# Kernel tuning notes

Measured on AMD Instinct MI355X. Metric: run time of the kernel, lower is better.

The kernel has to match this reference:

```python
import jax, jax.numpy as jnp
import numpy as np

B, H, W, N = 4, 64, 64, 64
NEAR, FAR = 2.0, 6.0
HID = 64


def setup_inputs() -> dict:
    key = jax.random.key(0)
    ks = jax.random.split(key, 6)
    ray_origins = jnp.tile(jnp.array([0.0, 0.0, 4.0], jnp.float32), (B, H, W, 1))
    ray_directions = jax.random.normal(ks[0], (B, H, W, 3), jnp.float32)
    tform_cam2world = jnp.eye(4, dtype=jnp.float32) + 0.1 * jax.random.normal(ks[1], (B, 4, 4), jnp.float32)
    depth_noise = jax.random.uniform(ks[2], (B, H, W, N), jnp.float32)
    u_samples = jax.random.uniform(ks[3], (B, H, W, N), jnp.float32)
    W1 = 0.5 * jax.random.normal(ks[4], (3, HID), jnp.float32)
    b1 = jnp.zeros((HID,), jnp.float32)
    W2 = 0.5 * jax.random.normal(ks[5], (HID, 4), jnp.float32)
    b2 = jnp.zeros((4,), jnp.float32)
    return dict(ray_origins=ray_origins, ray_directions=ray_directions,
                tform_cam2world=tform_cam2world, depth_noise=depth_noise,
                u_samples=u_samples, W1=W1, b1=b1, W2=W2, b2=b2)


def field(pts, W1, b1, W2, b2):
    # tiny radiance-field MLP standing in for the generator's sampler
    h = jax.nn.relu(pts @ W1 + b1)
    out = h @ W2 + b2
    sigma = out[..., 0]
    rgb = jax.nn.sigmoid(out[..., 1:4])
    return sigma, rgb


def compositing_weights(sigma, z_vals):
    # alpha-compositing weights (render_volume_density)
    dists = jnp.concatenate([z_vals[..., 1:] - z_vals[..., :-1],
                             jnp.full_like(z_vals[..., :1], 1e10)], axis=-1)
    alpha = 1.0 - jnp.exp(-jax.nn.relu(sigma) * dists)
    trans = jnp.cumprod(1.0 - alpha + 1e-10, axis=-1)
    trans = jnp.concatenate([jnp.ones_like(trans[..., :1]), trans[..., :-1]], axis=-1)
    return alpha * trans


def sample_pdf(bins, weights, u):
    # bins [R, M+1], weights [R, M], u [R, S] -> samples [R, S]
    pdf = weights / jnp.sum(weights, axis=-1, keepdims=True)
    cdf = jnp.cumsum(pdf, axis=-1)
    cdf = jnp.concatenate([jnp.zeros_like(cdf[..., :1]), cdf], axis=-1)  # [R, M+1]
    inds = jax.vmap(lambda c, uu: jnp.searchsorted(c, uu, side='right'))(cdf, u)
    last = cdf.shape[-1] - 1
    below = jnp.clip(inds - 1, 0, last)
    above = jnp.clip(inds, 0, last)
    cdf_b = jnp.take_along_axis(cdf, below, axis=-1)
    cdf_a = jnp.take_along_axis(cdf, above, axis=-1)
    bin_b = jnp.take_along_axis(bins, below, axis=-1)
    bin_a = jnp.take_along_axis(bins, above, axis=-1)
    denom = cdf_a - cdf_b
    denom = jnp.where(denom < 1e-5, 1.0, denom)
    t = (u - cdf_b) / denom
    return bin_b + t * (bin_a - bin_b)


def reference(ray_origins, ray_directions, tform_cam2world, depth_noise, u_samples, W1, b1, W2, b2):
    rd = ray_directions / jnp.linalg.norm(ray_directions, axis=-1, keepdims=True)
    # stratified coarse samples along each ray
    t = (jnp.arange(N, dtype=jnp.float32) + depth_noise) / N           # [B,H,W,N]
    z_vals = NEAR + (FAR - NEAR) * t
    pts = ray_origins[..., None, :] + rd[..., None, :] * z_vals[..., None]
    sigma, rgb = field(pts, W1, b1, W2, b2)                            # [B,H,W,N], [B,H,W,N,3]

    # --- hierarchical importance sampling (no_grad in original) ---
    w = compositing_weights(sigma, z_vals).reshape(-1, N)              # [R,N]
    pad = jnp.pad(w, ((0, 0), (1, 1)), constant_values=-jnp.inf)
    mx = jnp.maximum(pad[:, :-1], pad[:, 1:])                          # max_pool1d(k=2,s=1,p=1) -> [R,N+1]
    sm = 0.5 * (mx[:, :-1] + mx[:, 1:]) + 0.01                        # avg_pool1d(k=2,s=1)  -> [R,N]
    z_mid = (0.5 * (z_vals[..., 1:] + z_vals[..., :-1])).reshape(-1, N - 1)
    z_samples = sample_pdf(z_mid, sm[:, 1:-1], u_samples.reshape(-1, N))
    z_samples = jax.lax.stop_gradient(z_samples.reshape(B, H, W, N))

    # fine evaluation + merge-sort of coarse/fine samples
    z_all = jnp.concatenate([z_vals, z_samples], axis=-1)              # [B,H,W,2N]
    idx = jnp.argsort(z_all, axis=-1)
    z_sorted = jnp.take_along_axis(z_all, idx, axis=-1)
    pts_f = ray_origins[..., None, :] + rd[..., None, :] * z_samples[..., None]
    sigma_f, rgb_f = field(pts_f, W1, b1, W2, b2)
    sigma_all = jnp.take_along_axis(jnp.concatenate([sigma, sigma_f], axis=-1), idx, axis=-1)
    rgb_cat = jnp.concatenate([rgb, rgb_f], axis=-2)
    rgb_all = jnp.take_along_axis(rgb_cat, jnp.broadcast_to(idx[..., None], idx.shape + (3,)), axis=-2)

    # final alpha compositing
    w_all = compositing_weights(sigma_all, z_sorted)
    rgb_pred = jnp.sum(w_all[..., None] * rgb_all, axis=-2)            # [B,H,W,3]
    depth_pred = jnp.sum(w_all * z_sorted, axis=-1)                    # [B,H,W]
    mask_pred = jnp.sum(w_all, axis=-1)                                # [B,H,W]

    # camera-space depth (invert_space: R_w2c = R^T)
    R_w2c = jnp.swapaxes(tform_cam2world[:, :3, :3], -1, -2)           # [B,3,3]
    view_dir = jnp.einsum('bhwj,bij->bhwi', rd, R_w2c)
    depth_cam = -(view_dir * depth_pred[..., None])[..., -1]
    return rgb_pred, depth_cam, mask_pred
```

## Files before the change

kernel.cpp:

```cpp
#include <hip/hip_runtime.h>
#include <hip/hip_bf16.h>
#include <math.h>

#define Nn    64
#define RPB   2
#define NRAYS 16384
#define NEARV 2.0f
#define FARV  6.0f

typedef __attribute__((ext_vector_type(8))) short bf16x8;
typedef __attribute__((ext_vector_type(4))) float f32x4;
typedef __attribute__((ext_vector_type(2))) float f32x2;

template <int CTRL, int RMASK>
__device__ __forceinline__ float dpp_mv(float x, float ident) {
  return __int_as_float(__builtin_amdgcn_update_dpp(
      __float_as_int(ident), __float_as_int(x), CTRL, RMASK, 0xf, false));
}
__device__ __forceinline__ float shfl_up1(float x) {
  return __int_as_float(__builtin_amdgcn_update_dpp(
      __float_as_int(x), __float_as_int(x), 0x138, 0xf, 0xf, false));
}
__device__ __forceinline__ float shfl_dn1(float x) {
  return __int_as_float(__builtin_amdgcn_update_dpp(
      __float_as_int(x), __float_as_int(x), 0x130, 0xf, 0xf, false));
}
__device__ __forceinline__ float scan_add_dpp(float x) {
  x += dpp_mv<0x111, 0xf>(x, 0.f);
  x += dpp_mv<0x112, 0xf>(x, 0.f);
  x += dpp_mv<0x114, 0xf>(x, 0.f);
  x += dpp_mv<0x118, 0xf>(x, 0.f);
  x += dpp_mv<0x142, 0xa>(x, 0.f);
  x += dpp_mv<0x143, 0xc>(x, 0.f);
  return x;
}
__device__ __forceinline__ float scan_mul_dpp(float x) {
  x *= dpp_mv<0x111, 0xf>(x, 1.f);
  x *= dpp_mv<0x112, 0xf>(x, 1.f);
  x *= dpp_mv<0x114, 0xf>(x, 1.f);
  x *= dpp_mv<0x118, 0xf>(x, 1.f);
  x *= dpp_mv<0x142, 0xa>(x, 1.f);
  x *= dpp_mv<0x143, 0xc>(x, 1.f);
  return x;
}
__device__ __forceinline__ float reduce_add_bcast(float x) {
  x = scan_add_dpp(x);
  return __int_as_float(__builtin_amdgcn_readlane(__float_as_int(x), 63));
}

__device__ __forceinline__ float fast_rcp(float x) { return __builtin_amdgcn_rcpf(x); }
__device__ __forceinline__ float sigmoidf_fast(float x) { return fast_rcp(1.f + __expf(-x)); }

__device__ __forceinline__ short bfhi_bits(float x) { return (short)(__float_as_uint(x) >> 16); }
__device__ __forceinline__ float bfhi_val(float x)  { return __uint_as_float(__float_as_uint(x) & 0xFFFF0000u); }

template <int LEVEL, int D>
__device__ __forceinline__ void bitonic_stage(unsigned& k, int lane) {
  unsigned t;
  if constexpr (D == 32) {
    t = (unsigned)__builtin_amdgcn_ds_bpermute((lane ^ 32) << 2, (int)k);
  } else {
    t = (unsigned)__builtin_amdgcn_ds_swizzle((int)k, (D << 10) | 0x1F);
  }
  const bool bitd = (lane & D) != 0;
  const bool desc = (lane & (1 << LEVEL)) != 0;
  const unsigned mn = (k < t) ? k : t;
  const unsigned mx = (k < t) ? t : k;
  k = (bitd == desc) ? mn : mx;
}
template <int LEVEL, int D>
struct BSort {
  static __device__ __forceinline__ void run(unsigned& k, int lane) {
    bitonic_stage<LEVEL, D>(k, lane);
    if constexpr (D > 1) BSort<LEVEL, D / 2>::run(k, lane);
    else if constexpr (LEVEL < 6) BSort<LEVEL + 1, (1 << LEVEL)>::run(k, lane);
  }
};

template <int D>
__device__ __forceinline__ void merge_stage(unsigned& k, int lane) {
  unsigned t;
  if constexpr (D == 32) {
    t = (unsigned)__builtin_amdgcn_ds_bpermute((lane ^ 32) << 2, (int)k);
  } else {
    t = (unsigned)__builtin_amdgcn_ds_swizzle((int)k, (D << 10) | 0x1F);
  }
  const unsigned mn = (k < t) ? k : t;
  const unsigned mx = (k < t) ? t : k;
  k = ((lane & D) != 0) ? mx : mn;
}
__device__ __forceinline__ void merge64(unsigned& k, int lane) {
  merge_stage<32>(k, lane);
  merge_stage<16>(k, lane);
  merge_stage<8>(k, lane);
  merge_stage<4>(k, lane);
  merge_stage<2>(k, lane);
  merge_stage<1>(k, lane);
}

__device__ __forceinline__ int count_le_f(float arr, float x) {
  int cnt = 0;
#pragma unroll
  for (int step = 32; step >= 1; step >>= 1) {
    const int idx = cnt + step - 1;
    const float v = __shfl(arr, idx, 64);
    if (idx < 63 && v <= x) cnt += step;
  }
  return cnt;
}

template <bool SPLITB>
__device__ __forceinline__ void field_eval(
    float zlane, const f32x2 c0v[2][4], const f32x2 c1v[2][4],
    const bf16x8 aHi[2], const bf16x8 aLo[2],
    float b20, float b21, float b22, float b23,
    int quad, int col, float4* scratch, float o[4]) {
#pragma unroll
  for (int nt = 0; nt < 4; ++nt) {
    f32x4 acc = {0.f, 0.f, 0.f, 0.f};
    const float zm = __shfl(zlane, nt * 16 + col, 64);
    const f32x2 zm2 = {zm, zm};
#pragma unroll
    for (int ks = 0; ks < 2; ++ks) {
      union { bf16x8 v; unsigned u[4]; } Bhi, Blo;
#pragma unroll
      for (int p = 0; p < 4; ++p) {
        f32x2 h = zm2 * c1v[ks][p] + c0v[ks][p];
        h = __builtin_elementwise_max(h, (f32x2){0.f, 0.f});
        if constexpr (SPLITB) {
          union { f32x2 f; unsigned u[2]; } U; U.f = h;
          Bhi.u[p] = __builtin_amdgcn_perm(U.u[1], U.u[0], 0x07060302u);
          union { unsigned u[2]; f32x2 f; } M;
          M.u[0] = U.u[0] & 0xFFFF0000u;
          M.u[1] = U.u[1] & 0xFFFF0000u;
          const f32x2 l = h - M.f;
          union { f32x2 f; unsigned u[2]; } L; L.f = l;
          Blo.u[p] = __builtin_amdgcn_perm(L.u[1], L.u[0], 0x07060302u);
        } else {
          __hip_bfloat162 t = __float22bfloat162_rn(make_float2(h[0], h[1]));
          Bhi.u[p] = *reinterpret_cast<unsigned*>(&t);
        }
      }
      if constexpr (SPLITB) {
        acc = __builtin_amdgcn_mfma_f32_16x16x32_bf16(aHi[ks], Bhi.v, acc, 0, 0, 0);
        acc = __builtin_amdgcn_mfma_f32_16x16x32_bf16(aHi[ks], Blo.v, acc, 0, 0, 0);
        acc = __builtin_amdgcn_mfma_f32_16x16x32_bf16(aLo[ks], Bhi.v, acc, 0, 0, 0);
      } else {
        acc = __builtin_amdgcn_mfma_f32_16x16x32_bf16(aHi[ks], Bhi.v, acc, 0, 0, 0);
        acc = __builtin_amdgcn_mfma_f32_16x16x32_bf16(aLo[ks], Bhi.v, acc, 0, 0, 0);
      }
    }
    if (quad == 0) scratch[nt * 16 + col] = make_float4(acc[0], acc[1], acc[2], acc[3]);
  }
  const float4 r = scratch[(threadIdx.x & 63)];
  o[0] = r.x + b20; o[1] = r.y + b21; o[2] = r.z + b22; o[3] = r.w + b23;
}

__global__ __launch_bounds__(RPB * 64, 4) void nerf_fused(
    const float* __restrict__ ray_o, const float* __restrict__ ray_d,
    const float* __restrict__ tform, const float* __restrict__ noise,
    const float* __restrict__ usmp,  const float* __restrict__ W1,
    const float* __restrict__ b1,    const float* __restrict__ W2,
    const float* __restrict__ b2,    float* __restrict__ out) {
  const int wave = threadIdx.x >> 6;
  const int lane = threadIdx.x & 63;
  const int ray  = blockIdx.x * RPB + wave;
  const int quad = lane >> 4;
  const int col  = lane & 15;

  __shared__ float2 sC [RPB][Nn];
  __shared__ float4 sPk[RPB][2 * Nn];

  const float o0 = ray_o[ray * 3 + 0], o1 = ray_o[ray * 3 + 1], o2 = ray_o[ray * 3 + 2];
  float d0 = ray_d[ray * 3 + 0], d1 = ray_d[ray * 3 + 1], d2 = ray_d[ray * 3 + 2];
  const float rn = __builtin_amdgcn_rsqf(d0 * d0 + d1 * d1 + d2 * d2);
  d0 *= rn; d1 *= rn; d2 *= rn;

  {
    const float w10 = W1[lane], w11 = W1[64 + lane], w12 = W1[128 + lane];
    const float c1 = d0 * w10 + d1 * w11 + d2 * w12;
    const float c0 = o0 * w10 + o1 * w11 + o2 * w12 + b1[lane];
    sC[wave][lane] = make_float2(c0, c1);
  }

  const float nz = noise[ray * Nn + lane];
  const float z  = NEARV + (FARV - NEARV) * ((float)lane + nz) * (1.0f / Nn);
  const unsigned kc = ((__float_as_uint(z) - 0x40000000u) << 7) | (unsigned)lane;

  f32x2 c0v[2][4], c1v[2][4];
#pragma unroll
  for (int ks = 0; ks < 2; ++ks) {
    const float4* cc4 = (const float4*)&sC[wave][0];
    const int base4 = (ks * 32 + quad * 8) >> 1;
#pragma unroll
    for (int jj = 0; jj < 4; ++jj) {
      const float4 v = cc4[base4 + jj];
      c0v[ks][jj] = (f32x2){v.x, v.z};
      c1v[ks][jj] = (f32x2){v.y, v.w};
    }
  }

  bf16x8 aHi[2], aLo[2];
#pragma unroll
  for (int ks = 0; ks < 2; ++ks) {
#pragma unroll
    for (int j = 0; j < 8; ++j) {
      const int k = ks * 32 + quad * 8 + j;
      const float wv  = (col < 4) ? W2[k * 4 + col] : 0.f;
      aHi[ks][j] = bfhi_bits(wv);
      aLo[ks][j] = bfhi_bits(wv - bfhi_val(wv));
    }
  }
  const float b20 = b2[0], b21 = b2[1], b22 = b2[2], b23 = b2[3];
  float4* scratch = &sPk[wave][64];

  float oc[4];
  field_eval<true>(z, c0v, c1v, aHi, aLo, b20, b21, b22, b23, quad, col, scratch, oc);
  const float sig = oc[0];
  const float cr = sigmoidf_fast(oc[1]), cg = sigmoidf_fast(oc[2]), cb = sigmoidf_fast(oc[3]);
  sPk[wave][lane] = make_float4(sig, cr, cg, cb);

  const float zn   = shfl_dn1(z);
  const float dist = (lane == 63) ? 1e10f : (zn - z);
  const float alpha = 1.f - __expf(-fmaxf(sig, 0.f) * dist);
  float cdfreg, binreg;
  {
    const float P  = scan_mul_dpp(1.f - alpha + 1e-10f);
    float Te = shfl_up1(P);
    if (lane == 0) Te = 1.f;
    const float w = alpha * Te;

    const float mxA = fmaxf(shfl_up1(w), w);
    const float mxB = fmaxf(w, shfl_dn1(w));
    const float sm = 0.5f * (mxA + mxB) + 0.01f;

    const float v   = (lane >= 1 && lane <= 62) ? sm : 0.f;
    const float tot = reduce_add_bcast(v);
    const float pdf = v * fast_rcp(tot);
    const float C   = scan_add_dpp(pdf);
    cdfreg = (lane == 0) ? 0.f : C;
    binreg = 0.5f * (z + zn);
  }

  const float u = usmp[ray * Nn + lane];
  const int lo_i = count_le_f(cdfreg, u);
  const int below = lo_i - 1;
  const int above = (lo_i < 63) ? lo_i : 62;
  const float cdfb = __shfl(cdfreg, below, 64);
  const float cdfa = __shfl(cdfreg, above, 64);
  const float binb = __shfl(binreg, below, 64);
  const float bina = __shfl(binreg, above, 64);
  float den = cdfa - cdfb;
  if (den < 1e-5f) den = 1.f;
  const float zs = fmaf((u - cdfb) * fast_rcp(den), bina - binb, binb);

  const unsigned kf = ((__float_as_uint(zs) - 0x40000000u) << 7) | (unsigned)(64 + lane);
  unsigned kfS = kf;
  BSort<1, 1>::run(kfS, lane);

  float of[4];
  field_eval<false>(zs, c0v, c1v, aHi, aLo, b20, b21, b22, b23, quad, col, scratch, of);

  unsigned lok = kc;
  unsigned hik = (unsigned)__builtin_amdgcn_ds_bpermute((63 - lane) << 2, (int)kfS);
  {
    const unsigned mn = (lok < hik) ? lok : hik;
    const unsigned mx = (lok < hik) ? hik : lok;
    lok = mn; hik = mx;
  }
  merge64(lok, lane);
  merge64(hik, lane);

  const float sigF = of[0];
  const float fr = sigmoidf_fast(of[1]), fg = sigmoidf_fast(of[2]), fb = sigmoidf_fast(of[3]);
  sPk[wave][64 + lane] = make_float4(sigF, fr, fg, fb);

  const int a0 = ((2 * lane) & 63) << 2;
  const int a1 = ((2 * lane + 1) & 63) << 2;
  const unsigned l0 = (unsigned)__builtin_amdgcn_ds_bpermute(a0, (int)lok);
  const unsigned h0 = (unsigned)__builtin_amdgcn_ds_bpermute(a0, (int)hik);
  const unsigned l1 = (unsigned)__builtin_amdgcn_ds_bpermute(a1, (int)lok);
  const unsigned h1 = (unsigned)__builtin_amdgcn_ds_bpermute(a1, (int)hik);
  const unsigned k0 = (lane < 32) ? l0 : h0;
  const unsigned k1 = (lane < 32) ? l1 : h1;

  const float z0 = __uint_as_float((k0 >> 7) + 0x40000000u);
  const float z1 = __uint_as_float((k1 >> 7) + 0x40000000u);
  const float4 q0 = sPk[wave][k0 & 127u];
  const float4 q1 = sPk[wave][k1 & 127u];

  const float z2 = shfl_dn1(z0);
  const float dist0 = z1 - z0;
  const float dist1 = (lane == 63) ? 1e10f : (z2 - z1);
  const float al0 = 1.f - __expf(-fmaxf(q0.x, 0.f) * dist0);
  const float al1 = 1.f - __expf(-fmaxf(q1.x, 0.f) * dist1);
  const float aa0 = 1.f - al0 + 1e-10f;
  const float aa1 = 1.f - al1 + 1e-10f;
  const float Pp = scan_mul_dpp(aa0 * aa1);
  float Tp = shfl_up1(Pp);
  if (lane == 0) Tp = 1.f;
  const float w0 = al0 * Tp;
  const float w1 = al1 * Tp * aa0;

  const float accR = reduce_add_bcast(w0 * q0.y + w1 * q1.y);
  const float accG = reduce_add_bcast(w0 * q0.z + w1 * q1.z);
  const float accB = reduce_add_bcast(w0 * q0.w + w1 * q1.w);
  const float accD = reduce_add_bcast(w0 * z0 + w1 * z1);
  const float accM = reduce_add_bcast(w0 + w1);

  if (lane == 0) {
    const float* tf = tform + (ray >> 12) * 16;
    const float vz = d0 * tf[2] + d1 * tf[6] + d2 * tf[10];
    out[ray * 3 + 0]     = accR;
    out[ray * 3 + 1]     = accG;
    out[ray * 3 + 2]     = accB;
    out[NRAYS * 3 + ray] = -vz * accD;
    out[NRAYS * 4 + ray] = accM;
  }
}

extern "C" void kernel_launch(void* const* d_in, const int* in_sizes, int n_in,
                              void* d_out, int out_size, void* d_ws, size_t ws_size,
                              hipStream_t stream) {
  const float* ray_o = (const float*)d_in[0];
  const float* ray_d = (const float*)d_in[1];
  const float* tform = (const float*)d_in[2];
  const float* noise = (const float*)d_in[3];
  const float* usmp  = (const float*)d_in[4];
  const float* W1    = (const float*)d_in[5];
  const float* b1    = (const float*)d_in[6];
  const float* W2    = (const float*)d_in[7];
  const float* b2    = (const float*)d_in[8];
  float* out = (float*)d_out;

  nerf_fused<<<dim3(NRAYS / RPB), RPB * 64, 0, stream>>>(
      ray_o, ray_d, tform, noise, usmp, W1, b1, W2, b2, out);
}
```

Before: 101.9 us.

## Replace bitonic sort and merge with rank-based scatter using sorted uniforms

Sorts the uniform samples up front so the inverse-CDF samples come out monotone, then computes each fine sample's insertion position among the coarse samples directly from the searchsorted bin. A shared-memory histogram with atomics plus an integer DPP prefix scan gives the coarse positions. Both key sets are scattered into shared memory instead of running the bitonic sort on fine keys and two merge networks. It still sorts the uniforms (one bitonic pass) and adds LDS atomics and scatter traffic. It relies on sorted-u giving sorted z_samples, which holds mathematically for the monotone CDF.

```diff
diff --git a/kernel.cpp b/kernel.cpp
--- a/kernel.cpp
+++ b/kernel.cpp
@@ -16,6 +16,10 @@
 __device__ __forceinline__ float dpp_mv(float x, float ident) {
   return __int_as_float(__builtin_amdgcn_update_dpp(
       __float_as_int(ident), __float_as_int(x), CTRL, RMASK, 0xf, false));
+}
+template <int CTRL, int RMASK>
+__device__ __forceinline__ int dpp_mvi(int x, int ident) {
+  return __builtin_amdgcn_update_dpp(ident, x, CTRL, RMASK, 0xf, false);
 }
 __device__ __forceinline__ float shfl_up1(float x) {
   return __int_as_float(__builtin_amdgcn_update_dpp(
@@ -34,6 +38,15 @@
   x += dpp_mv<0x143, 0xc>(x, 0.f);
   return x;
 }
+__device__ __forceinline__ int scan_add_dpp_int(int x) {
+  x += dpp_mvi<0x111, 0xf>(x, 0);
+  x += dpp_mvi<0x112, 0xf>(x, 0);
+  x += dpp_mvi<0x114, 0xf>(x, 0);
+  x += dpp_mvi<0x118, 0xf>(x, 0);
+  x += dpp_mvi<0x142, 0xa>(x, 0);
+  x += dpp_mvi<0x143, 0xc>(x, 0);
+  return x;
+}
 __device__ __forceinline__ float scan_mul_dpp(float x) {
   x *= dpp_mv<0x111, 0xf>(x, 1.f);
   x *= dpp_mv<0x112, 0xf>(x, 1.f);
@@ -76,27 +89,6 @@
     else if constexpr (LEVEL < 6) BSort<LEVEL + 1, (1 << LEVEL)>::run(k, lane);
   }
 };
-
-template <int D>
-__device__ __forceinline__ void merge_stage(unsigned& k, int lane) {
-  unsigned t;
-  if constexpr (D == 32) {
-    t = (unsigned)__builtin_amdgcn_ds_bpermute((lane ^ 32) << 2, (int)k);
-  } else {
-    t = (unsigned)__builtin_amdgcn_ds_swizzle((int)k, (D << 10) | 0x1F);
-  }
-  const unsigned mn = (k < t) ? k : t;
-  const unsigned mx = (k < t) ? t : k;
-  k = ((lane & D) != 0) ? mx : mn;
-}
-__device__ __forceinline__ void merge64(unsigned& k, int lane) {
-  merge_stage<32>(k, lane);
-  merge_stage<16>(k, lane);
-  merge_stage<8>(k, lane);
-  merge_stage<4>(k, lane);
-  merge_stage<2>(k, lane);
-  merge_stage<1>(k, lane);
-}
 
 __device__ __forceinline__ int count_le_f(float arr, float x) {
   int cnt = 0;
@@ -168,8 +160,12 @@
   const int quad = lane >> 4;
   const int col  = lane & 15;
 
-  __shared__ float2 sC [RPB][Nn];
-  __shared__ float4 sPk[RPB][2 * Nn];
+  __shared__ float2   sC  [RPB][Nn];
+  __shared__ float4   sPk [RPB][2 * Nn];
+  __shared__ unsigned sKey[RPB][2 * Nn];
+  __shared__ unsigned sHist[RPB][Nn];
+
+  sHist[wave][lane] = 0u;
 
   const float o0 = ray_o[ray * 3 + 0], o1 = ray_o[ray * 3 + 1], o2 = ray_o[ray * 3 + 2];
   float d0 = ray_d[ray * 3 + 0], d1 = ray_d[ray * 3 + 1], d2 = ray_d[ray * 3 + 2];
@@ -186,6 +182,10 @@
   const float nz = noise[ray * Nn + lane];
   const float z  = NEARV + (FARV - NEARV) * ((float)lane + nz) * (1.0f / Nn);
   const unsigned kc = ((__float_as_uint(z) - 0x40000000u) << 7) | (unsigned)lane;
+
+  unsigned ub = __float_as_uint(usmp[ray * Nn + lane]);
+  BSort<1, 1>::run(ub, lane);
+  const float us = __uint_as_float(ub);
 
   f32x2 c0v[2][4], c1v[2][4];
 #pragma unroll
@@ -242,8 +242,7 @@
     binreg = 0.5f * (z + zn);
   }
 
-  const float u = usmp[ray * Nn + lane];
-  const int lo_i = count_le_f(cdfreg, u);
+  const int lo_i = count_le_f(cdfreg, us);
   const int below = lo_i - 1;
   const int above = (lo_i < 63) ? lo_i : 62;
   const float cdfb = __shfl(cdfreg, below, 64);
@@ -252,37 +251,31 @@
   const float bina = __shfl(binreg, above, 64);
   float den = cdfa - cdfb;
   if (den < 1e-5f) den = 1.f;
-  const float zs = fmaf((u - cdfb) * fast_rcp(den), bina - binb, binb);
-
+  const float zs = fmaf((us - cdfb) * fast_rcp(den), bina - binb, binb);
+
+  const float zb1 = __shfl(z, below + 1, 64);
+  const int   cj  = below + 1 + ((zb1 <= zs) ? 1 : 0);
+  const int   pos_f = lane + cj;
   const unsigned kf = ((__float_as_uint(zs) - 0x40000000u) << 7) | (unsigned)(64 + lane);
-  unsigned kfS = kf;
-  BSort<1, 1>::run(kfS, lane);
+
+  atomicAdd(&sHist[wave][cj], 1u);
 
   float of[4];
   field_eval<false>(zs, c0v, c1v, aHi, aLo, b20, b21, b22, b23, quad, col, scratch, of);
 
-  unsigned lok = kc;
-  unsigned hik = (unsigned)__builtin_amdgcn_ds_bpermute((63 - lane) << 2, (int)kfS);
-  {
-    const unsigned mn = (lok < hik) ? lok : hik;
-    const unsigned mx = (lok < hik) ? hik : lok;
-    lok = mn; hik = mx;
-  }
-  merge64(lok, lane);
-  merge64(hik, lane);
+  const int h    = (int)sHist[wave][lane];
+  const int pref = scan_add_dpp_int(h);
+  const int pos_c = lane + pref;
 
   const float sigF = of[0];
   const float fr = sigmoidf_fast(of[1]), fg = sigmoidf_fast(of[2]), fb = sigmoidf_fast(of[3]);
   sPk[wave][64 + lane] = make_float4(sigF, fr, fg, fb);
 
-  const int a0 = ((2 * lane) & 63) << 2;
-  const int a1 = ((2 * lane + 1) & 63) << 2;
-  const unsigned l0 = (unsigned)__builtin_amdgcn_ds_bpermute(a0, (int)lok);
-  const unsigned h0 = (unsigned)__builtin_amdgcn_ds_bpermute(a0, (int)hik);
-  const unsigned l1 = (unsigned)__builtin_amdgcn_ds_bpermute(a1, (int)lok);
-  const unsigned h1 = (unsigned)__builtin_amdgcn_ds_bpermute(a1, (int)hik);
-  const unsigned k0 = (lane < 32) ? l0 : h0;
-  const unsigned k1 = (lane < 32) ? l1 : h1;
+  sKey[wave][pos_c] = kc;
+  sKey[wave][pos_f] = kf;
+  const uint2 kk = *reinterpret_cast<const uint2*>(&sKey[wave][2 * lane]);
+  const unsigned k0 = kk.x;
+  const unsigned k1 = kk.y;
 
   const float z0 = __uint_as_float((k0 >> 7) + 0x40000000u);
   const float z1 = __uint_as_float((k1 >> 7) + 0x40000000u);
```

Result: no change. 102.7 us (+0.8%).
